# Optimization experiments

Measured on AMD Instinct MI355X. Metric: run time of the kernel, lower is better.

Reference implementation:

```python
import jax, jax.numpy as jnp
import numpy as np

F, S, D, W = 64, 8192, 128, 128   # fields (batch*heads), seq_len, head_dim, n_waves
MAX_SEQ = 8192
ALPHA = 0.1
TWO_PI = 2.0 * np.pi


def setup_inputs() -> dict:
    key = jax.random.key(0)
    k1, k2, k3, k4 = jax.random.split(key, 4)
    kv_vectors = jax.random.normal(k1, (F, S, D), dtype=jnp.float32)
    positions = jnp.arange(S, dtype=jnp.int32)
    # per-field linear weights (torch Linear stores [out, in])
    W_enc = jax.random.normal(k2, (F, 3 * W, D), dtype=jnp.float32) / np.float32(np.sqrt(D))
    W_dec = jax.random.normal(k3, (F, D, W), dtype=jnp.float32) / np.float32(np.sqrt(W))
    # base_freqs ~ linspace(0.1, 10.0) in torch; sample uniformly in that range per field
    base_freqs = 0.1 + 9.9 * jax.random.uniform(k4, (F, W), dtype=jnp.float32)
    return {"kv_vectors": kv_vectors, "positions": positions,
            "W_enc": W_enc, "W_dec": W_dec, "base_freqs": base_freqs}


def reference(kv_vectors, positions, W_enc, W_dec, base_freqs):
    # encode: [F,S,D] x [F,3W,D] -> [F,S,3W]
    deltas = jnp.einsum('fsd,fkd->fsk', kv_vectors, W_enc)
    d_freq, d_amp, d_phase = jnp.split(deltas, 3, axis=-1)   # each [F,S,W]

    pos_norm = positions.astype(jnp.float32) / MAX_SEQ        # [S]
    pos_signal = jnp.sin(TWO_PI * base_freqs[:, None, :] * pos_norm[None, :, None])  # [F,S,W]

    # EMA recurrence s_t = (1-a) s_{t-1} + a x_t from zero init has closed form:
    # s_S = sum_t a * (1-a)^(S-1-t) * x_t  -> single weighted reduction over S.
    log1ma = np.float32(np.log1p(-ALPHA))
    w = ALPHA * jnp.exp(jnp.arange(S - 1, -1, -1, dtype=jnp.float32) * log1ma)  # [S]

    freqs = jnp.einsum('s,fsw->fw', w, d_freq * pos_signal)
    amps = jnp.einsum('s,fsw->fw', w, jnp.abs(d_amp))
    phases = jnp.einsum('s,fsw->fw', w, d_phase)

    # reconstruct at the same positions: [F,S,W]
    wave_phases = TWO_PI * (freqs + base_freqs)[:, None, :] * pos_norm[None, :, None] + phases[:, None, :]
    wave_values = amps[:, None, :] * jnp.sin(wave_phases)
    # decode: [F,S,W] x [F,D,W] -> [F,S,D]
    return jnp.einsum('fsw,fdw->fsd', wave_values, W_dec)
```

## Files before the change

### kernel.cpp

```cpp
#include <hip/hip_runtime.h>
#include <hip/hip_bf16.h>

#define NF 64
#define NS 8192
#define ND 128
#define NW 128
#define NK3 384
#define TKEEP 128
#define SBASE (NS - TKEEP)

typedef __attribute__((ext_vector_type(4))) float f32x4;
typedef __attribute__((ext_vector_type(8))) short bf16x8;

__device__ __forceinline__ short f2bf(float x) {
    union { float f; unsigned u; } v; v.f = x;
    unsigned r = v.u + 0x7FFFu + ((v.u >> 16) & 1u);
    return (short)(r >> 16);
}
__device__ __forceinline__ float bf2f(short b) {
    union { float f; unsigned u; } v;
    v.u = ((unsigned)(unsigned short)b) << 16;
    return v.f;
}
__device__ __forceinline__ float sin2pi(float t) {
    return __builtin_amdgcn_sinf(t - floorf(t));
}

__global__ __launch_bounds__(256) void wf_wdec(
    const float* __restrict__ Wdec,
    short* __restrict__ wdf)
{
    const int f = blockIdx.x;
    const int c = blockIdx.y * 256 + threadIdx.x;
    const int nt = c >> 8;
    const int ks = (c >> 6) & 3;
    const int ln = c & 63;
    const int row = nt * 16 + (ln & 15);
    const int col = ks * 32 + ((ln >> 4) << 3);
    const float* src = Wdec + ((size_t)f * ND + row) * NW + col;
    f32x4 a = *(const f32x4*)src;
    f32x4 b = *(const f32x4*)(src + 4);
    bf16x8 p;
    p[0] = f2bf(a[0]); p[1] = f2bf(a[1]); p[2] = f2bf(a[2]); p[3] = f2bf(a[3]);
    p[4] = f2bf(b[0]); p[5] = f2bf(b[1]); p[6] = f2bf(b[2]); p[7] = f2bf(b[3]);
    *(bf16x8*)(wdf + ((size_t)f * 2048 + c) * 8) = p;
}

__global__ __launch_bounds__(256) void wf_stage_a(
    const float* __restrict__ kv,
    const float* __restrict__ Wenc,
    const float* __restrict__ bfreq,
    float* __restrict__ wpar)
{
    const int f    = blockIdx.x;
    const int kb   = blockIdx.y;
    const int tid  = threadIdx.x;
    const int lane = tid & 63;
    const int wv   = tid >> 6;
    const int rgrp = lane >> 4;
    const int rlo  = lane & 15;

    const int nt = kb * 4 + wv;
    const int kg = nt * 16 + rlo;

    __shared__ short kvhi[TKEEP * ND];
    __shared__ short kvlo[TKEEP * ND];
    __shared__ float wgt[TKEEP];

    f32x4 wA[4], wB[4];
    #pragma unroll
    for (int ks = 0; ks < 4; ++ks) {
        const float* srcW = Wenc + ((size_t)f * NK3 + kg) * ND + ks * 32 + rgrp * 8;
        wA[ks] = *(const f32x4*)srcW;
        wB[ks] = *(const f32x4*)(srcW + 4);
    }

    {
        int c   = tid & 15;
        int sr0 = tid >> 4;
        #pragma unroll
        for (int r = 0; r < 8; ++r) {
            int s = sr0 + 16 * r;
            const float* src = kv + ((size_t)f * NS + SBASE + s) * ND + c * 8;
            f32x4 a = *(const f32x4*)src;
            f32x4 b = *(const f32x4*)(src + 4);
            bf16x8 hi, lo;
            #pragma unroll
            for (int j = 0; j < 4; ++j) {
                short h = f2bf(a[j]); hi[j] = h; lo[j] = f2bf(a[j] - bf2f(h));
            }
            #pragma unroll
            for (int j = 0; j < 4; ++j) {
                short h = f2bf(b[j]); hi[4 + j] = h; lo[4 + j] = f2bf(b[j] - bf2f(h));
            }
            int ofs = s * ND + ((c * 8) ^ ((s & 7) << 3));
            *(bf16x8*)(kvhi + ofs) = hi;
            *(bf16x8*)(kvlo + ofs) = lo;
        }
        if (tid < TKEEP)
            wgt[tid] = 0.1f * expf((float)(TKEEP - 1 - tid) * (-0.10536051565782628f));
    }
    __syncthreads();

    f32x4 acc[8];
    #pragma unroll
    for (int m = 0; m < 8; ++m) acc[m] = (f32x4){0.f, 0.f, 0.f, 0.f};

    #pragma unroll
    for (int ks = 0; ks < 4; ++ks) {
        bf16x8 bhi, blo;
        #pragma unroll
        for (int q = 0; q < 4; ++q) {
            short h = f2bf(wA[ks][q]); bhi[q] = h; blo[q] = f2bf(wA[ks][q] - bf2f(h));
        }
        #pragma unroll
        for (int q = 0; q < 4; ++q) {
            short h = f2bf(wB[ks][q]); bhi[4 + q] = h; blo[4 + q] = f2bf(wB[ks][q] - bf2f(h));
        }
        int colBase = ks * 32 + rgrp * 8;
        #pragma unroll
        for (int m = 0; m < 8; ++m) {
            int row = m * 16 + rlo;
            int ofs = row * ND + (colBase ^ ((row & 7) << 3));
            bf16x8 ahi = *(const bf16x8*)(kvhi + ofs);
            bf16x8 alo = *(const bf16x8*)(kvlo + ofs);
            acc[m] = __builtin_amdgcn_mfma_f32_16x16x32_bf16(ahi, bhi, acc[m], 0, 0, 0);
            acc[m] = __builtin_amdgcn_mfma_f32_16x16x32_bf16(alo, bhi, acc[m], 0, 0, 0);
            acc[m] = __builtin_amdgcn_mfma_f32_16x16x32_bf16(ahi, blo, acc[m], 0, 0, 0);
        }
    }

    float bfv = (nt < 8) ? bfreq[f * NW + kg] : 0.f;
    float psum = 0.f;
    #pragma unroll
    for (int m = 0; m < 8; ++m) {
        #pragma unroll
        for (int r = 0; r < 4; ++r) {
            int sl = m * 16 + rgrp * 4 + r;
            float v = acc[m][r];
            if (nt < 8) {
                float posn = (float)(SBASE + sl) * (1.0f / 8192.0f);
                v *= sin2pi(bfv * posn);
            } else if (nt < 16) {
                v = fabsf(v);
            }
            psum += v * wgt[sl];
        }
    }
    psum += __shfl_xor(psum, 16);
    psum += __shfl_xor(psum, 32);
    if (rgrp == 0) {
        if (nt < 8)       wpar[f * NW + kg] = psum + bfv;
        else if (nt < 16) wpar[8192 + f * NW + (kg - 128)] = psum;
        else              wpar[16384 + f * NW + (kg - 256)] = psum * 0.15915494309189535f;
    }
}

__global__ __launch_bounds__(256) void wf_stage_b(
    const float* __restrict__ wpar,
    const short* __restrict__ wdf,
    float* __restrict__ out)
{
    const int st   = blockIdx.x;
    const int f    = blockIdx.y;
    const int tid  = threadIdx.x;
    const int lane = tid & 63;
    const int wv   = tid >> 6;
    const int wr   = wv >> 1;
    const int wc   = wv & 1;
    const int rgrp = lane >> 4;
    const int rlo  = lane & 15;

    __shared__ short waveLDS[128 * NW];
    __shared__ float pLDS[384];

    if (tid < 96) {
        int a  = tid >> 5;
        int i4 = (tid & 31) * 4;
        *(f32x4*)&pLDS[a * 128 + i4] = *(const f32x4*)&wpar[a * 8192 + f * NW + i4];
    }
    __syncthreads();

    {
        int srow = tid & 127;
        int half = tid >> 7;
        float posn = (float)(st * 128 + srow) * (1.0f / 8192.0f);
        #pragma unroll
        for (int c = 0; c < 8; ++c) {
            int w0 = half * 64 + c * 8;
            f32x4 fa = *(const f32x4*)&pLDS[w0];
            f32x4 fb = *(const f32x4*)&pLDS[w0 + 4];
            f32x4 aa = *(const f32x4*)&pLDS[128 + w0];
            f32x4 ab = *(const f32x4*)&pLDS[128 + w0 + 4];
            f32x4 pa = *(const f32x4*)&pLDS[256 + w0];
            f32x4 pb = *(const f32x4*)&pLDS[256 + w0 + 4];
            bf16x8 pk;
            #pragma unroll
            for (int j = 0; j < 4; ++j)
                pk[j] = f2bf(aa[j] * sin2pi(fa[j] * posn + pa[j]));
            #pragma unroll
            for (int j = 0; j < 4; ++j)
                pk[4 + j] = f2bf(ab[j] * sin2pi(fb[j] * posn + pb[j]));
            *(bf16x8*)&waveLDS[srow * NW + (w0 ^ ((srow & 7) << 3))] = pk;
        }
    }
    __syncthreads();

    f32x4 acc[4][4];
    #pragma unroll
    for (int mi = 0; mi < 4; ++mi)
        #pragma unroll
        for (int ni = 0; ni < 4; ++ni)
            acc[mi][ni] = (f32x4){0.f, 0.f, 0.f, 0.f};

    const short* wdfF = wdf + (size_t)f * 16384;
    #pragma unroll
    for (int ks = 0; ks < 4; ++ks) {
        bf16x8 bfr[4];
        #pragma unroll
        for (int ni = 0; ni < 4; ++ni) {
            int nt = wc * 4 + ni;
            bfr[ni] = *(const bf16x8*)(wdfF + ((size_t)((nt * 4 + ks) * 64 + lane)) * 8);
        }
        bf16x8 afr[4];
        #pragma unroll
        for (int mi = 0; mi < 4; ++mi) {
            int row = wr * 64 + mi * 16 + rlo;
            int col = ks * 32 + rgrp * 8;
            afr[mi] = *(const bf16x8*)&waveLDS[row * NW + (col ^ ((row & 7) << 3))];
        }
        #pragma unroll
        for (int mi = 0; mi < 4; ++mi)
            #pragma unroll
            for (int ni = 0; ni < 4; ++ni)
                acc[mi][ni] = __builtin_amdgcn_mfma_f32_16x16x32_bf16(afr[mi], bfr[ni], acc[mi][ni], 0, 0, 0);
    }

    size_t base = ((size_t)f * NS + (size_t)st * 128) * ND;
    #pragma unroll
    for (int mi = 0; mi < 4; ++mi) {
        #pragma unroll
        for (int r = 0; r < 4; ++r) {
            int sl = wr * 64 + mi * 16 + rgrp * 4 + r;
            float* dst = out + base + (size_t)sl * ND + wc * 64 + rlo;
            #pragma unroll
            for (int ni = 0; ni < 4; ++ni)
                dst[ni * 16] = acc[mi][ni][r];
        }
    }
}

extern "C" void kernel_launch(void* const* d_in, const int* in_sizes, int n_in,
                              void* d_out, int out_size, void* d_ws, size_t ws_size,
                              hipStream_t stream) {
    const float* kv    = (const float*)d_in[0];
    const float* Wenc  = (const float*)d_in[2];
    const float* Wdec  = (const float*)d_in[3];
    const float* bfreq = (const float*)d_in[4];

    float* wpar = (float*)d_ws;
    short* wdf  = (short*)((char*)d_ws + 98304);

    wf_wdec   <<<dim3(NF, 8), 256, 0, stream>>>(Wdec, wdf);
    wf_stage_a<<<dim3(NF, 6), 256, 0, stream>>>(kv, Wenc, bfreq, wpar);
    wf_stage_b<<<dim3(NS / 128, NF), 256, 0, stream>>>(wpar, wdf, (float*)d_out);
}
```

Measured before the change: 403.3 us.

## Generate wave fragments in registers, transpose MFMA for vector stores, fold W_dec pack

Stage B no longer builds the wave matrix in LDS. Each wave computes its sine values straight into MFMA B-operand registers, and the GEMM is transposed (W_dec as A) so the accumulators can be written as contiguous float4 rows. This removes the LDS round trip and a barrier, and lets the launch-bounds hint of 3 raise occupancy. The separate W_dec bf16 packing kernel is merged into stage A to save a launch. The cost is some sine work repeated across the waves that share a column group.

```diff
diff --git a/kernel.cpp b/kernel.cpp
--- a/kernel.cpp
+++ b/kernel.cpp
@@ -26,31 +26,13 @@
     return __builtin_amdgcn_sinf(t - floorf(t));
 }
 
-__global__ __launch_bounds__(256) void wf_wdec(
-    const float* __restrict__ Wdec,
-    short* __restrict__ wdf)
-{
-    const int f = blockIdx.x;
-    const int c = blockIdx.y * 256 + threadIdx.x;
-    const int nt = c >> 8;
-    const int ks = (c >> 6) & 3;
-    const int ln = c & 63;
-    const int row = nt * 16 + (ln & 15);
-    const int col = ks * 32 + ((ln >> 4) << 3);
-    const float* src = Wdec + ((size_t)f * ND + row) * NW + col;
-    f32x4 a = *(const f32x4*)src;
-    f32x4 b = *(const f32x4*)(src + 4);
-    bf16x8 p;
-    p[0] = f2bf(a[0]); p[1] = f2bf(a[1]); p[2] = f2bf(a[2]); p[3] = f2bf(a[3]);
-    p[4] = f2bf(b[0]); p[5] = f2bf(b[1]); p[6] = f2bf(b[2]); p[7] = f2bf(b[3]);
-    *(bf16x8*)(wdf + ((size_t)f * 2048 + c) * 8) = p;
-}
-
 __global__ __launch_bounds__(256) void wf_stage_a(
     const float* __restrict__ kv,
     const float* __restrict__ Wenc,
+    const float* __restrict__ Wdec,
     const float* __restrict__ bfreq,
-    float* __restrict__ wpar)
+    float* __restrict__ wpar,
+    short* __restrict__ wdf)
 {
     const int f    = blockIdx.x;
     const int kb   = blockIdx.y;
@@ -73,6 +55,25 @@
         const float* srcW = Wenc + ((size_t)f * NK3 + kg) * ND + ks * 32 + rgrp * 8;
         wA[ks] = *(const f32x4*)srcW;
         wB[ks] = *(const f32x4*)(srcW + 4);
+    }
+
+    if (kb < 4) {
+        #pragma unroll
+        for (int i = 0; i < 2; ++i) {
+            int c = kb * 512 + i * 256 + tid;
+            int cnt = c >> 8;
+            int cks = (c >> 6) & 3;
+            int ln  = c & 63;
+            int row = cnt * 16 + (ln & 15);
+            int col = cks * 32 + ((ln >> 4) << 3);
+            const float* src = Wdec + ((size_t)f * ND + row) * NW + col;
+            f32x4 a = *(const f32x4*)src;
+            f32x4 b = *(const f32x4*)(src + 4);
+            bf16x8 p;
+            p[0] = f2bf(a[0]); p[1] = f2bf(a[1]); p[2] = f2bf(a[2]); p[3] = f2bf(a[3]);
+            p[4] = f2bf(b[0]); p[5] = f2bf(b[1]); p[6] = f2bf(b[2]); p[7] = f2bf(b[3]);
+            *(bf16x8*)(wdf + ((size_t)f * 2048 + c) * 8) = p;
+        }
     }
 
     {
@@ -156,7 +157,7 @@
     }
 }
 
-__global__ __launch_bounds__(256) void wf_stage_b(
+__global__ __launch_bounds__(256, 3) void wf_stage_b(
     const float* __restrict__ wpar,
     const short* __restrict__ wdf,
     float* __restrict__ out)
@@ -171,7 +172,6 @@
     const int rgrp = lane >> 4;
     const int rlo  = lane & 15;
 
-    __shared__ short waveLDS[128 * NW];
     __shared__ float pLDS[384];
 
     if (tid < 96) {
@@ -181,72 +181,56 @@
     }
     __syncthreads();
 
-    {
-        int srow = tid & 127;
-        int half = tid >> 7;
-        float posn = (float)(st * 128 + srow) * (1.0f / 8192.0f);
-        #pragma unroll
-        for (int c = 0; c < 8; ++c) {
-            int w0 = half * 64 + c * 8;
-            f32x4 fa = *(const f32x4*)&pLDS[w0];
-            f32x4 fb = *(const f32x4*)&pLDS[w0 + 4];
-            f32x4 aa = *(const f32x4*)&pLDS[128 + w0];
-            f32x4 ab = *(const f32x4*)&pLDS[128 + w0 + 4];
-            f32x4 pa = *(const f32x4*)&pLDS[256 + w0];
-            f32x4 pb = *(const f32x4*)&pLDS[256 + w0 + 4];
-            bf16x8 pk;
+    f32x4 acc[4][4];
+    #pragma unroll
+    for (int di = 0; di < 4; ++di)
+        #pragma unroll
+        for (int si = 0; si < 4; ++si)
+            acc[di][si] = (f32x4){0.f, 0.f, 0.f, 0.f};
+
+    const short* wdfF = wdf + (size_t)f * 16384;
+    const float sb = (float)(st * 128 + wc * 64 + rlo);
+
+    #pragma unroll
+    for (int ks = 0; ks < 4; ++ks) {
+        bf16x8 afr[4];
+        #pragma unroll
+        for (int di = 0; di < 4; ++di) {
+            int nt = wr * 4 + di;
+            afr[di] = *(const bf16x8*)(wdfF + ((size_t)((nt * 4 + ks) * 64 + lane)) * 8);
+        }
+        int w0 = ks * 32 + rgrp * 8;
+        f32x4 fa = *(const f32x4*)&pLDS[w0];
+        f32x4 fb = *(const f32x4*)&pLDS[w0 + 4];
+        f32x4 aa = *(const f32x4*)&pLDS[128 + w0];
+        f32x4 ab = *(const f32x4*)&pLDS[128 + w0 + 4];
+        f32x4 pa = *(const f32x4*)&pLDS[256 + w0];
+        f32x4 pb = *(const f32x4*)&pLDS[256 + w0 + 4];
+        bf16x8 bw[4];
+        #pragma unroll
+        for (int si = 0; si < 4; ++si) {
+            float posn = (sb + (float)(si * 16)) * (1.0f / 8192.0f);
             #pragma unroll
             for (int j = 0; j < 4; ++j)
-                pk[j] = f2bf(aa[j] * sin2pi(fa[j] * posn + pa[j]));
+                bw[si][j] = f2bf(aa[j] * sin2pi(fa[j] * posn + pa[j]));
             #pragma unroll
             for (int j = 0; j < 4; ++j)
-                pk[4 + j] = f2bf(ab[j] * sin2pi(fb[j] * posn + pb[j]));
-            *(bf16x8*)&waveLDS[srow * NW + (w0 ^ ((srow & 7) << 3))] = pk;
-        }
-    }
-    __syncthreads();
-
-    f32x4 acc[4][4];
-    #pragma unroll
-    for (int mi = 0; mi < 4; ++mi)
-        #pragma unroll
-        for (int ni = 0; ni < 4; ++ni)
-            acc[mi][ni] = (f32x4){0.f, 0.f, 0.f, 0.f};
-
-    const short* wdfF = wdf + (size_t)f * 16384;
-    #pragma unroll
-    for (int ks = 0; ks < 4; ++ks) {
-        bf16x8 bfr[4];
-        #pragma unroll
-        for (int ni = 0; ni < 4; ++ni) {
-            int nt = wc * 4 + ni;
-            bfr[ni] = *(const bf16x8*)(wdfF + ((size_t)((nt * 4 + ks) * 64 + lane)) * 8);
-        }
-        bf16x8 afr[4];
-        #pragma unroll
-        for (int mi = 0; mi < 4; ++mi) {
-            int row = wr * 64 + mi * 16 + rlo;
-            int col = ks * 32 + rgrp * 8;
-            afr[mi] = *(const bf16x8*)&waveLDS[row * NW + (col ^ ((row & 7) << 3))];
-        }
-        #pragma unroll
-        for (int mi = 0; mi < 4; ++mi)
-            #pragma unroll
-            for (int ni = 0; ni < 4; ++ni)
-                acc[mi][ni] = __builtin_amdgcn_mfma_f32_16x16x32_bf16(afr[mi], bfr[ni], acc[mi][ni], 0, 0, 0);
+                bw[si][4 + j] = f2bf(ab[j] * sin2pi(fb[j] * posn + pb[j]));
+        }
+        #pragma unroll
+        for (int di = 0; di < 4; ++di)
+            #pragma unroll
+            for (int si = 0; si < 4; ++si)
+                acc[di][si] = __builtin_amdgcn_mfma_f32_16x16x32_bf16(afr[di], bw[si], acc[di][si], 0, 0, 0);
     }
 
     size_t base = ((size_t)f * NS + (size_t)st * 128) * ND;
     #pragma unroll
-    for (int mi = 0; mi < 4; ++mi) {
-        #pragma unroll
-        for (int r = 0; r < 4; ++r) {
-            int sl = wr * 64 + mi * 16 + rgrp * 4 + r;
-            float* dst = out + base + (size_t)sl * ND + wc * 64 + rlo;
-            #pragma unroll
-            for (int ni = 0; ni < 4; ++ni)
-                dst[ni * 16] = acc[mi][ni][r];
-        }
+    for (int si = 0; si < 4; ++si) {
+        size_t rowOff = base + (size_t)(wc * 64 + si * 16 + rlo) * ND + wr * 64 + rgrp * 4;
+        #pragma unroll
+        for (int di = 0; di < 4; ++di)
+            *(f32x4*)(out + rowOff + di * 16) = acc[di][si];
     }
 }
 
@@ -261,7 +245,6 @@
     float* wpar = (float*)d_ws;
     short* wdf  = (short*)((char*)d_ws + 98304);
 
-    wf_wdec   <<<dim3(NF, 8), 256, 0, stream>>>(Wdec, wdf);
-    wf_stage_a<<<dim3(NF, 6), 256, 0, stream>>>(kv, Wenc, bfreq, wpar);
+    wf_stage_a<<<dim3(NF, 6), 256, 0, stream>>>(kv, Wenc, Wdec, bfreq, wpar, wdf);
     wf_stage_b<<<dim3(NS / 128, NF), 256, 0, stream>>>(wpar, wdf, (float*)d_out);
 }
```

Result: slower. 415.5 us (+3.0%).
